# Kernel tuning notes

Measured on AMD Instinct MI355X. Metric: run time of the kernel, lower is better.

## Reference

```python
import jax, jax.numpy as jnp
import numpy as np

B, T, C = 2, 2048, 1024
H = 16
HD = C // H  # 64


def setup_inputs() -> dict:
    key = jax.random.key(0)
    k1, k2, k3, k4, k5 = jax.random.split(key, 5)
    s = 0.02
    return {
        "x": jax.random.normal(k1, (B, T, C), dtype=jnp.float32),
        "w_attn": jax.random.normal(k2, (C, 3 * C), dtype=jnp.float32) * s,
        "b_attn": jnp.zeros((3 * C,), dtype=jnp.float32),
        "w_proj": jax.random.normal(k3, (C, C), dtype=jnp.float32) * s,
        "b_proj": jnp.zeros((C,), dtype=jnp.float32),
    }


def reference(x, w_attn, b_attn, w_proj, b_proj):
    Bx, Tx, Cx = x.shape
    qkv = x @ w_attn + b_attn                      # [B,T,3C]
    q, k, v = jnp.split(qkv, 3, axis=-1)
    # [B,T,C] -> [B,H,T,HD]
    def heads(t):
        return t.reshape(Bx, Tx, H, HD).transpose(0, 2, 1, 3)
    q, k, v = heads(q), heads(k), heads(v)
    scale = 1.0 / np.sqrt(HD).astype(np.float32)
    scores = jnp.einsum("bhqd,bhkd->bhqk", q, k) * scale
    causal = jnp.tril(jnp.ones((Tx, Tx), dtype=bool))
    scores = jnp.where(causal, scores, -jnp.inf)
    attn = jax.nn.softmax(scores, axis=-1)          # dropout p=0 -> identity
    y = jnp.einsum("bhqk,bhkd->bhqd", attn, v)
    y = y.transpose(0, 2, 1, 3).reshape(Bx, Tx, Cx)
    return y @ w_proj + b_proj
```

## Files before the change

kernel.cpp:

```cpp
#include <hip/hip_runtime.h>
#include <hip/hip_bf16.h>

#define Bb 2
#define Tt 2048
#define Cc 1024
#define Hh 16
#define HD 64
#define QS 0.18033688f

typedef __attribute__((ext_vector_type(8))) short bf16x8;
typedef __attribute__((ext_vector_type(4))) short bf16x4;
typedef __attribute__((ext_vector_type(4))) float f32x4;
typedef __attribute__((ext_vector_type(2))) unsigned int u32x2;

__device__ inline short f2b(float f) {
    unsigned int u = __builtin_bit_cast(unsigned int, f);
    unsigned int r = (u + 0x7FFFu + ((u >> 16) & 1u)) >> 16;
    return (short)(unsigned short)r;
}

__device__ inline void gl16(const void* g, void* l) {
    __builtin_amdgcn_global_load_lds(
        (const __attribute__((address_space(1))) void*)g,
        (__attribute__((address_space(3))) void*)l, 16, 0, 0);
}

__global__ __launch_bounds__(256) void prep_kernel(
    const float* __restrict__ x, short* __restrict__ xbf,
    const float* __restrict__ wA, short* __restrict__ wAT,
    const float* __restrict__ wP, short* __restrict__ wPT)
{
    const int bx = blockIdx.x, tid = threadIdx.x;
    if (bx < 2048) {
        int i = (bx * 256 + tid) * 8;
        float4 a = *(const float4*)(x + i);
        float4 b = *(const float4*)(x + i + 4);
        bf16x8 v;
        v[0] = f2b(a.x); v[1] = f2b(a.y); v[2] = f2b(a.z); v[3] = f2b(a.w);
        v[4] = f2b(b.x); v[5] = f2b(b.y); v[6] = f2b(b.z); v[7] = f2b(b.w);
        *(bf16x8*)(xbf + i) = v;
        return;
    }
    const float* W; short* WT; int N, t;
    if (bx < 2816) { t = bx - 2048; W = wA; WT = wAT; N = 3072; }
    else           { t = bx - 2816; W = wP; WT = wPT; N = 1024; }
    const int K = 1024;
    int k0 = (t & 15) * 64, n0 = (t >> 4) * 64;
    int nl = tid & 63, kg = tid >> 6;
    int n = n0 + nl;
    short v[16];
#pragma unroll
    for (int i = 0; i < 16; i++)
        v[i] = f2b(W[(size_t)(k0 + kg * 16 + i) * N + n]);
    short* dst = WT + (size_t)n * K + k0 + kg * 16;
    *(bf16x8*)dst = *(bf16x8*)&v[0];
    *(bf16x8*)(dst + 8) = *(bf16x8*)&v[8];
}

#define VM0 asm volatile("s_waitcnt vmcnt(0)" ::: "memory")
#define BARRIER asm volatile("s_barrier" ::: "memory")
#define SCHEDB __builtin_amdgcn_sched_barrier(0)

#define STG(nb, kb) { \
    gl16(A + baA0 + (kb), &LB[((nb) << 1) * 4096 + dst8]); \
    gl16(A + baA0 + 32768 + (kb), &LB[((nb) << 1) * 4096 + 2048 + dst8]); \
    gl16(A + baA1 + (kb), &LB[(((nb) << 1) | 1) * 4096 + dst8]); \
    gl16(A + baA1 + 32768 + (kb), &LB[(((nb) << 1) | 1) * 4096 + 2048 + dst8]); \
    gl16(Bt + baB0 + (kb), &LB[16384 + ((nb) << 1) * 4096 + dst8]); \
    gl16(Bt + baB0 + 32768 + (kb), &LB[16384 + ((nb) << 1) * 4096 + 2048 + dst8]); \
    gl16(Bt + baB1 + (kb), &LB[16384 + (((nb) << 1) | 1) * 4096 + dst8]); \
    gl16(Bt + baB1 + 32768 + (kb), &LB[16384 + (((nb) << 1) | 1) * 4096 + 2048 + dst8]); }

#define RD_A(bb, flo) { \
    const short* Ab_ = &LB[(((bb) << 1) | wm) * 4096]; \
    _Pragma("unroll") for (int f_ = 0; f_ < 2; f_++) \
        _Pragma("unroll") for (int kh_ = 0; kh_ < 2; kh_++) \
            af[(flo) + f_][kh_] = *(const bf16x8*)&Ab_[aro[(flo) + f_] + kx[kh_]]; }

#define RD_B(bb, elo) { \
    const short* Bb_ = &LB[16384 + (((bb) << 1) | wn) * 4096]; \
    _Pragma("unroll") for (int e_ = 0; e_ < 2; e_++) \
        _Pragma("unroll") for (int kh_ = 0; kh_ < 2; kh_++) \
            bf[(elo) + e_][kh_] = *(const bf16x8*)&Bb_[bro[(elo) + e_] + kx[kh_]]; }

#define QMM(FH, EH) { \
    __builtin_amdgcn_s_setprio(1); \
    _Pragma("unroll") for (int f_ = 0; f_ < 2; f_++) \
        _Pragma("unroll") for (int e_ = 0; e_ < 2; e_++) \
            _Pragma("unroll") for (int kh_ = 0; kh_ < 2; kh_++) \
                acc[(FH) * 2 + f_][(EH) * 2 + e_] = \
                    __builtin_amdgcn_mfma_f32_16x16x32_bf16( \
                        af[(FH) * 2 + f_][kh_], bf[(EH) * 2 + e_][kh_], \
                        acc[(FH) * 2 + f_][(EH) * 2 + e_], 0, 0, 0); \
    __builtin_amdgcn_s_setprio(0); }

#define TILE(bb, nb, kb1) { \
    RD_A(bb, 0); RD_B(bb, 0); \
    STG(nb, kb1); \
    QMM(0, 0); \
    RD_B(bb, 2); QMM(0, 1); \
    RD_A(bb, 2); QMM(1, 1); \
    QMM(1, 0); \
    VM0; BARRIER; SCHEDB; }

#define TILE_LAST(bb) { \
    RD_A(bb, 0); RD_B(bb, 0); \
    QMM(0, 0); \
    RD_B(bb, 2); QMM(0, 1); \
    RD_A(bb, 2); QMM(1, 1); \
    QMM(1, 0); }

__global__ __launch_bounds__(256, 2) void gemm_qkv(
    const short* __restrict__ A, const short* __restrict__ Bt,
    const float* __restrict__ bias,
    short* __restrict__ qw, short* __restrict__ kw, short* __restrict__ vTw,
    int M, int N, int K)
{
    __shared__ __attribute__((aligned(16))) short LB[32768];

    const int tid  = threadIdx.x;
    const int wave = tid >> 6, lane = tid & 63;
    const int quad = lane >> 4, lr = lane & 15;
    const int wm = wave >> 1, wn = wave & 1;

    const int bid = blockIdx.x;
    const int sw = (bid & 7) * 96 + (bid >> 3);
    const int bx = sw % 24, by = sw / 24;
    const int m0 = by * 128, n0 = bx * 128;

    const int dst8 = tid * 8;
    const int cs = ((tid & 7) ^ ((tid >> 3) & 7)) << 3;
    const size_t baA0 = (size_t)(m0 + (tid >> 3)) * 1024 + cs;
    const size_t baA1 = (size_t)(m0 + 64 + (tid >> 3)) * 1024 + cs;
    const size_t baB0 = (size_t)(n0 + (tid >> 3)) * 1024 + cs;
    const size_t baB1 = (size_t)(n0 + 64 + (tid >> 3)) * 1024 + cs;

    int aro[4], bro[4], kx[2];
#pragma unroll
    for (int f = 0; f < 4; f++) {
        aro[f] = (f * 16 + lr) * 64;
        bro[f] = (f * 16 + lr) * 64;
    }
#pragma unroll
    for (int kh = 0; kh < 2; kh++)
        kx[kh] = (((kh * 4 + quad) ^ (lr & 7)) << 3);

    f32x4 acc[4][4];
    const f32x4 zf = {0.f, 0.f, 0.f, 0.f};
#pragma unroll
    for (int mf = 0; mf < 4; mf++)
#pragma unroll
        for (int nf = 0; nf < 4; nf++) acc[mf][nf] = zf;

    bf16x8 af[4][2], bf[4][2];

    STG(0, 0);
    VM0;
    BARRIER;

    for (int it = 0; it < 7; ++it) {
        TILE(0, 1, (2 * it + 1) << 6);
        TILE(1, 0, (2 * it + 2) << 6);
    }
    TILE(0, 1, 15 << 6);
    TILE_LAST(1);

    if (n0 < 2048) {
#pragma unroll
        for (int nf = 0; nf < 4; nf++) {
#pragma unroll
            for (int mf = 0; mf < 4; mf++) {
                int c = n0 + wn * 64 + nf * 16 + lr;
                float bv = bias[c];
#pragma unroll
                for (int r = 0; r < 4; r++) {
                    int rg = m0 + wm * 64 + mf * 16 + quad * 4 + r;
                    float val = acc[mf][nf][r] + bv;
                    int which = c >> 10, cc = c & 1023;
                    int h = cc >> 6, d = cc & 63;
                    int b = rg >> 11, t = rg & 2047;
                    size_t bh = (size_t)b * Hh + h;
                    if (which == 0) qw[(bh * Tt + t) * HD + d] = f2b(val * QS);
                    else            kw[(bh * Tt + t) * HD + d] = f2b(val);
                }
            }
        }
    } else {
        __syncthreads();
#pragma unroll
        for (int nf = 0; nf < 4; nf++) {
            int cl = wn * 64 + nf * 16 + lr;
            float bv = bias[n0 + cl];
#pragma unroll
            for (int mf = 0; mf < 4; mf++)
#pragma unroll
                for (int r = 0; r < 4; r++) {
                    int tl = wm * 64 + mf * 16 + quad * 4 + r;
                    LB[cl * 136 + tl] = f2b(acc[mf][nf][r] + bv);
                }
        }
        __syncthreads();
        const int rl = tid >> 1, half = tid & 1;
        const int cc = (n0 & 1023) + rl;
        const int h = cc >> 6, d = cc & 63;
        const int b = m0 >> 11, tb = (m0 & 2047) + half * 64;
        short* dst = vTw + (((size_t)b * Hh + h) * HD + d) * Tt + tb;
        const short* src = &LB[rl * 136 + half * 64];
#pragma unroll
        for (int jj = 0; jj < 8; jj++)
            *(bf16x8*)(dst + jj * 8) = *(const bf16x8*)(src + jj * 8);
    }
}

__global__ __launch_bounds__(256) void gemm_proj(
    const short* __restrict__ A, const short* __restrict__ Bt,
    const float* __restrict__ bias, float* __restrict__ out,
    int M, int N, int K)
{
    __shared__ __attribute__((aligned(16))) short SH[12288];

    const int tid  = threadIdx.x;
    const int wave = tid >> 6, lane = tid & 63;
    const int quad = lane >> 4, lr = lane & 15;
    const int wm = wave >> 1, wn = wave & 1;
    const int m0 = blockIdx.y * 64, n0 = blockIdx.x * 128;

    const int arow = tid >> 2;
    const int acol = ((tid & 3) ^ ((arow >> 1) & 3)) << 3;
    int brow[2], bcol[2];
#pragma unroll
    for (int i = 0; i < 2; i++) {
        int id = i * 256 + tid;
        brow[i] = id >> 2;
        bcol[i] = ((id & 3) ^ ((brow[i] >> 1) & 3)) << 3;
    }
    const int pfrag = quad ^ ((lr >> 1) & 3);

    f32x4 acc[2][4];
    const f32x4 zf = {0.f, 0.f, 0.f, 0.f};
#pragma unroll
    for (int mi = 0; mi < 2; mi++)
#pragma unroll
        for (int ni = 0; ni < 4; ni++) acc[mi][ni] = zf;

    auto asrc = [&](int row, int col) -> const short* {
        int rg = m0 + row, b = rg >> 11, t = rg & 2047;
        int h = col >> 6, d = col & 63;
        return A + ((((size_t)b * Hh + h) * Tt + t) * HD + d);
    };

    gl16(asrc(arow, acol), &SH[tid * 8]);
#pragma unroll
    for (int i = 0; i < 2; i++)
        gl16(Bt + (size_t)(n0 + brow[i]) * K + bcol[i],
             &SH[4096 + (i * 256 + tid) * 8]);

    const int iters = K >> 5;
    for (int it = 0; it < iters; ++it) {
        const int coA = (it & 1) * 2048, noA = ((it & 1) ^ 1) * 2048;
        const int coB = (it & 1) * 4096, noB = ((it & 1) ^ 1) * 4096;
        __syncthreads();
        if (it + 1 < iters) {
            const int k1 = (it + 1) << 5;
            gl16(asrc(arow, k1 + acol), &SH[noA + tid * 8]);
#pragma unroll
            for (int i = 0; i < 2; i++)
                gl16(Bt + (size_t)(n0 + brow[i]) * K + k1 + bcol[i],
                     &SH[4096 + noB + (i * 256 + tid) * 8]);
        }
        bf16x8 af[2], bf[4];
#pragma unroll
        for (int mi = 0; mi < 2; mi++) {
            int row = wm * 32 + mi * 16 + lr;
            af[mi] = *(bf16x8*)&SH[coA + (row * 4 + pfrag) * 8];
        }
#pragma unroll
        for (int ni = 0; ni < 4; ni++) {
            int row = wn * 64 + ni * 16 + lr;
            bf[ni] = *(bf16x8*)&SH[4096 + coB + (row * 4 + pfrag) * 8];
        }
#pragma unroll
        for (int mi = 0; mi < 2; mi++)
#pragma unroll
            for (int ni = 0; ni < 4; ni++)
                acc[mi][ni] = __builtin_amdgcn_mfma_f32_16x16x32_bf16(
                    af[mi], bf[ni], acc[mi][ni], 0, 0, 0);
    }

#pragma unroll
    for (int mi = 0; mi < 2; mi++)
#pragma unroll
        for (int ni = 0; ni < 4; ni++) {
            int c = n0 + wn * 64 + ni * 16 + lr;
            float bv = bias[c];
#pragma unroll
            for (int r = 0; r < 4; r++) {
                int rg = m0 + wm * 32 + mi * 16 + quad * 4 + r;
                out[(size_t)rg * N + c] = acc[mi][ni][r] + bv;
            }
        }
}

__global__ __launch_bounds__(256) void gemm_f32src(
    const void* __restrict__ Araw, const float* __restrict__ Bm,
    const float* __restrict__ bias, float* __restrict__ out,
    short* __restrict__ qw, short* __restrict__ kw, short* __restrict__ vTw,
    int M, int N, int K, int mode)
{
    __shared__ __attribute__((aligned(16))) short As[128 * 32];
    __shared__ __attribute__((aligned(16))) short Bs[128 * 32];

    const int tid  = threadIdx.x;
    const int wave = tid >> 6, lane = tid & 63;
    const int quad = lane >> 4, lr = lane & 15;
    const int wm = wave >> 1, wn = wave & 1;
    const int m0 = blockIdx.y * 128, n0 = blockIdx.x * 128;

    f32x4 acc[4][4];
    const f32x4 zf = {0.f, 0.f, 0.f, 0.f};
#pragma unroll
    for (int mi = 0; mi < 4; mi++)
#pragma unroll
        for (int ni = 0; ni < 4; ni++) acc[mi][ni] = zf;

    for (int k0 = 0; k0 < K; k0 += 32) {
        __syncthreads();
        if (mode == 1) {
            const float* Af = (const float*)Araw;
#pragma unroll
            for (int i = 0; i < 4; i++) {
                int id  = i * 256 + tid;
                int row = id >> 3;
                int kc  = (id & 7) << 2;
                float4 v = *(const float4*)(Af + (size_t)(m0 + row) * K + k0 + kc);
                short* d = &As[row * 32 + kc];
                d[0] = f2b(v.x); d[1] = f2b(v.y); d[2] = f2b(v.z); d[3] = f2b(v.w);
            }
        } else {
            const short* Ah = (const short*)Araw;
#pragma unroll
            for (int i = 0; i < 2; i++) {
                int id  = i * 256 + tid;
                int row = id >> 2;
                int kc  = (id & 3) << 3;
                int rg = m0 + row, b = rg >> 11, t = rg & 2047;
                int c = k0 + kc, h = c >> 6, d = c & 63;
                *(bf16x8*)&As[row * 32 + kc] =
                    *(const bf16x8*)(Ah + ((((size_t)b * Hh + h) * Tt + t) * HD + d));
            }
        }
#pragma unroll
        for (int i = 0; i < 4; i++) {
            int id = i * 256 + tid;
            int kr = id >> 5;
            int nc = (id & 31) << 2;
            float4 v = *(const float4*)(Bm + (size_t)(k0 + kr) * N + n0 + nc);
            Bs[(nc + 0) * 32 + kr] = f2b(v.x);
            Bs[(nc + 1) * 32 + kr] = f2b(v.y);
            Bs[(nc + 2) * 32 + kr] = f2b(v.z);
            Bs[(nc + 3) * 32 + kr] = f2b(v.w);
        }
        __syncthreads();

        bf16x8 af[4], bf[4];
#pragma unroll
        for (int mi = 0; mi < 4; mi++)
            af[mi] = *(bf16x8*)&As[(wm * 64 + mi * 16 + lr) * 32 + quad * 8];
#pragma unroll
        for (int ni = 0; ni < 4; ni++)
            bf[ni] = *(bf16x8*)&Bs[(wn * 64 + ni * 16 + lr) * 32 + quad * 8];
#pragma unroll
        for (int mi = 0; mi < 4; mi++)
#pragma unroll
            for (int ni = 0; ni < 4; ni++)
                acc[mi][ni] = __builtin_amdgcn_mfma_f32_16x16x32_bf16(
                    af[mi], bf[ni], acc[mi][ni], 0, 0, 0);
    }

#pragma unroll
    for (int mi = 0; mi < 4; mi++) {
#pragma unroll
        for (int ni = 0; ni < 4; ni++) {
            int c = n0 + wn * 64 + ni * 16 + lr;
            float bv = bias[c];
#pragma unroll
            for (int r = 0; r < 4; r++) {
                int rg = m0 + wm * 64 + mi * 16 + quad * 4 + r;
                float val = acc[mi][ni][r] + bv;
                if (mode == 1) {
                    int which = c >> 10, cc = c & 1023;
                    int h = cc >> 6, d = cc & 63;
                    int b = rg >> 11, t = rg & 2047;
                    size_t bh = (size_t)b * Hh + h;
                    if (which == 0)      qw[(bh * Tt + t) * HD + d] = f2b(val * QS);
                    else if (which == 1) kw[(bh * Tt + t) * HD + d] = f2b(val);
                    else                 vTw[(bh * HD + d) * Tt + t] = f2b(val);
                } else {
                    out[(size_t)rg * N + c] = val;
                }
            }
        }
    }
}

__global__ __launch_bounds__(256) void attn_kernel(
    short* __restrict__ qw, const short* __restrict__ kw,
    const short* __restrict__ vTw)
{
    __shared__ __attribute__((aligned(16))) short Ks[2][8192];
    __shared__ __attribute__((aligned(16))) short Vs[2][8192];

    const int bh = blockIdx.x & 31;
    const int g  = blockIdx.x >> 5;
    const int tid = threadIdx.x;
    const int wave = tid >> 6, lane = tid & 63;
    const int quad = lane >> 4, lr = lane & 15;

    const int pA = 2 * g + (wave >> 1);
    const int pB = 63 - pA;
    const int wh = (wave & 1) * 16;
    const int r0m[2] = { pA * 32 + wh, pB * 32 + wh };

    short* qp = qw + (size_t)bh * Tt * HD;
    const short* kp = kw + (size_t)bh * Tt * HD;
    const short* vp = vTw + (size_t)bh * HD * Tt;

    int krow[4], kcol[4], vrow[4], vcol[4];
#pragma unroll
    for (int i = 0; i < 4; i++) {
        int id = i * 256 + tid;
        krow[i] = id >> 3;
        kcol[i] = ((id & 7) ^ (krow[i] & 7)) << 3;
        vrow[i] = id >> 4;
        vcol[i] = ((id & 15) ^ (vrow[i] & 15)) << 3;
    }

    const int kb0b = lr * 64 + ((quad     ^ (lr & 7)) << 3);
    const int kb1b = lr * 64 + (((4 + quad) ^ (lr & 7)) << 3);
    const int qh = quad >> 1, ql = quad & 1;
    int vbase[4];
#pragma unroll
    for (int nt = 0; nt < 4; nt++)
        vbase[nt] = (nt * 16 + lr) * 128 + ql * 4;

    bf16x8 aq[2][2];
#pragma unroll
    for (int mt = 0; mt < 2; mt++)
#pragma unroll
        for (int h = 0; h < 2; h++)
            aq[mt][h] = *(const bf16x8*)(qp + (size_t)(r0m[mt] + lr) * HD
                                            + h * 32 + quad * 8);

    const f32x4 zf = {0.f, 0.f, 0.f, 0.f};
    f32x4 o[2][4];
    float lacc[2] = {0.f, 0.f};
#pragma unroll
    for (int mt = 0; mt < 2; mt++)
#pragma unroll
        for (int nt = 0; nt < 4; nt++) o[mt][nt] = zf;

#pragma unroll
    for (int i = 0; i < 4; i++) {
        gl16(kp + (size_t)krow[i] * HD + kcol[i], &Ks[0][(i * 256 + tid) * 8]);
        gl16(vp + (size_t)vrow[i] * Tt + vcol[i], &Vs[0][(i * 256 + tid) * 8]);
    }

    const int clast = ((63 - 2 * g) * 32 + 31) >> 7;
    for (int c = 0; c <= clast; ++c) {
        const int j0 = c << 7;
        const int cur = c & 1;
        __syncthreads();
        if (c < clast) {
#pragma unroll
            for (int i = 0; i < 4; i++) {
                gl16(kp + (size_t)(j0 + 128 + krow[i]) * HD + kcol[i],
                     &Ks[cur ^ 1][(i * 256 + tid) * 8]);
                gl16(vp + (size_t)vrow[i] * Tt + (j0 + 128) + vcol[i],
                     &Vs[cur ^ 1][(i * 256 + tid) * 8]);
            }
        }
        const short* Kc = &Ks[cur][0];
        const short* Vc = &Vs[cur][0];
        __builtin_amdgcn_s_setprio(1);
#pragma unroll
        for (int kt = 0; kt < 8; kt++) {
            const int k16 = j0 + kt * 16;
            const bool act0 = k16 <= r0m[0] + 15;
            const bool act1 = k16 <= r0m[1] + 15;
            if (!act1 && !act0) break;
            bf16x8 kb0 = *(const bf16x8*)&Kc[kt * 1024 + kb0b];
            bf16x8 kb1 = *(const bf16x8*)&Kc[kt * 1024 + kb1b];
            const int sl8 = (((kt * 2 + qh) ^ lr) << 3);
            bf16x4 va[4];
#pragma unroll
            for (int nt = 0; nt < 4; nt++)
                va[nt] = *(const bf16x4*)&Vc[vbase[nt] + sl8];
#pragma unroll
            for (int mt = 0; mt < 2; mt++) {
                if (!(mt ? act1 : act0)) continue;
                f32x4 s = __builtin_amdgcn_mfma_f32_16x16x32_bf16(
                    kb0, aq[mt][0], zf, 0, 0, 0);
                s = __builtin_amdgcn_mfma_f32_16x16x32_bf16(
                    kb1, aq[mt][1], s, 0, 0, 0);
                unsigned u[4];
                if (k16 + 15 <= r0m[mt]) {
#pragma unroll
                    for (int r = 0; r < 4; r++) {
                        float e = __builtin_amdgcn_exp2f(s[r]);
                        u[r] = __builtin_bit_cast(unsigned, e);
                        lacc[mt] += e;
                    }
                } else {
#pragma unroll
                    for (int r = 0; r < 4; r++) {
                        float e = __builtin_amdgcn_exp2f(s[r]);
                        if ((k16 + quad * 4 + r) > (r0m[mt] + lr)) e = 0.f;
                        u[r] = __builtin_bit_cast(unsigned, e);
                        lacc[mt] += e;
                    }
                }
                u32x2 pu = { __builtin_amdgcn_perm(u[1], u[0], 0x07060302u),
                             __builtin_amdgcn_perm(u[3], u[2], 0x07060302u) };
                bf16x4 pt = __builtin_bit_cast(bf16x4, pu);
#pragma unroll
                for (int nt = 0; nt < 4; nt++)
                    o[mt][nt] = __builtin_amdgcn_mfma_f32_16x16x16bf16_1k(
                        va[nt], pt, o[mt][nt], 0, 0, 0);
            }
        }
        __builtin_amdgcn_s_setprio(0);
    }

#pragma unroll
    for (int mt = 0; mt < 2; mt++) {
        lacc[mt] += __shfl_xor(lacc[mt], 16, 64);
        lacc[mt] += __shfl_xor(lacc[mt], 32, 64);
        lacc[mt] = 1.0f / lacc[mt];
    }

#pragma unroll
    for (int mt = 0; mt < 2; mt++)
#pragma unroll
        for (int nt = 0; nt < 4; nt++) {
            bf16x4 ov;
#pragma unroll
            for (int r = 0; r < 4; r++) ov[r] = f2b(o[mt][nt][r] * lacc[mt]);
            *(bf16x4*)(qp + (size_t)(r0m[mt] + lr) * HD + nt * 16 + quad * 4) = ov;
        }
}

extern "C" void kernel_launch(void* const* d_in, const int* in_sizes, int n_in,
                              void* d_out, int out_size, void* d_ws, size_t ws_size,
                              hipStream_t stream) {
    const float* x      = (const float*)d_in[0];
    const float* w_attn = (const float*)d_in[1];
    const float* b_attn = (const float*)d_in[2];
    const float* w_proj = (const float*)d_in[3];
    const float* b_proj = (const float*)d_in[4];
    float* out = (float*)d_out;

    const size_t per = (size_t)Bb * Hh * Tt * HD;
    short* qw  = (short*)d_ws;
    short* kw  = qw + per;
    short* vTw = kw + per;
    const int M = Bb * Tt;

    const size_t need_fast = (3 * per + per + (size_t)3072 * 1024 + (size_t)1024 * 1024) * 2;

    if (ws_size >= need_fast) {
        short* xbf = vTw + per;
        short* wAT = xbf + per;
        short* wPT = wAT + (size_t)3072 * 1024;

        prep_kernel<<<dim3(3072), 256, 0, stream>>>(x, xbf, w_attn, wAT, w_proj, wPT);

        gemm_qkv<<<dim3(768), 256, 0, stream>>>(
            xbf, wAT, b_attn, qw, kw, vTw, M, 3 * Cc, Cc);

        attn_kernel<<<dim3(512), 256, 0, stream>>>(qw, kw, vTw);

        gemm_proj<<<dim3(Cc / 128, M / 64), 256, 0, stream>>>(
            qw, wPT, b_proj, out, M, Cc, Cc);
    } else {
        gemm_f32src<<<dim3(3 * Cc / 128, M / 128), 256, 0, stream>>>(
            x, w_attn, b_attn, nullptr, qw, kw, vTw, M, 3 * Cc, Cc, 1);

        attn_kernel<<<dim3(512), 256, 0, stream>>>(qw, kw, vTw);

        gemm_f32src<<<dim3(Cc / 128, M / 128), 256, 0, stream>>>(
            qw, w_proj, b_proj, out, nullptr, nullptr, nullptr, M, Cc, Cc, 2);
    }
}
```

Measured before the change: 174.9 us.

## Split attention key tiles across two wave groups and pipeline proj GEMM with K=64 tiles

The attention kernel now runs 512 threads per block: two groups of four waves each handle half of every 128-key chunk. Their partial outputs and row sums are combined through shared memory at the end. This doubles the waves per query tile, aiming to cut per-wave serial latency, at the cost of a final reduction and fewer load instructions per thread. The projection GEMM is rewritten to use K=64 tiles in a macro-driven double-buffered loop with interleaved LDS reads and MFMAs, priority hints and launch_bounds(256,2), which trades more shared memory for fewer barriers.

Result: no change. 171.5 us (-1.9%).

```diff
diff --git a/kernel.cpp b/kernel.cpp
--- a/kernel.cpp
+++ b/kernel.cpp
@@ -212,12 +212,55 @@
     }
 }
 
-__global__ __launch_bounds__(256) void gemm_proj(
+#define P_STG(nb, kb) { \
+    gl16(A + baA0 + (size_t)(kb) * 2048, &LB[(nb) * 4096 + dst8]); \
+    gl16(A + baA1 + (size_t)(kb) * 2048, &LB[(nb) * 4096 + 2048 + dst8]); \
+    gl16(Bt + baB0 + (kb), &LB[8192 + (nb) * 8192 + dst8]); \
+    gl16(Bt + baB1 + (kb), &LB[8192 + (nb) * 8192 + 2048 + dst8]); \
+    gl16(Bt + baB2 + (kb), &LB[8192 + (nb) * 8192 + 4096 + dst8]); \
+    gl16(Bt + baB3 + (kb), &LB[8192 + (nb) * 8192 + 6144 + dst8]); }
+
+#define P_RDA(bb) { \
+    const short* Ab_ = &LB[(bb) * 4096]; \
+    _Pragma("unroll") for (int f_ = 0; f_ < 2; f_++) \
+        _Pragma("unroll") for (int kh_ = 0; kh_ < 2; kh_++) \
+            af[f_][kh_] = *(const bf16x8*)&Ab_[aro[f_] + kx[kh_]]; }
+
+#define P_RDB(bb, elo) { \
+    const short* Bb_ = &LB[8192 + (bb) * 8192]; \
+    _Pragma("unroll") for (int e_ = 0; e_ < 2; e_++) \
+        _Pragma("unroll") for (int kh_ = 0; kh_ < 2; kh_++) \
+            bf[(elo) + e_][kh_] = *(const bf16x8*)&Bb_[bro[(elo) + e_] + kx[kh_]]; }
+
+#define P_QMM(EH) { \
+    __builtin_amdgcn_s_setprio(1); \
+    _Pragma("unroll") for (int f_ = 0; f_ < 2; f_++) \
+        _Pragma("unroll") for (int e_ = 0; e_ < 2; e_++) \
+            _Pragma("unroll") for (int kh_ = 0; kh_ < 2; kh_++) \
+                acc[f_][(EH) * 2 + e_] = \
+                    __builtin_amdgcn_mfma_f32_16x16x32_bf16( \
+                        af[f_][kh_], bf[(EH) * 2 + e_][kh_], \
+                        acc[f_][(EH) * 2 + e_], 0, 0, 0); \
+    __builtin_amdgcn_s_setprio(0); }
+
+#define P_TILE(bb, nb, kb1) { \
+    P_RDA(bb); P_RDB(bb, 0); \
+    P_STG(nb, kb1); \
+    P_QMM(0); \
+    P_RDB(bb, 2); P_QMM(1); \
+    VM0; BARRIER; SCHEDB; }
+
+#define P_TILE_LAST(bb) { \
+    P_RDA(bb); P_RDB(bb, 0); \
+    P_QMM(0); \
+    P_RDB(bb, 2); P_QMM(1); }
+
+__global__ __launch_bounds__(256, 2) void gemm_proj(
     const short* __restrict__ A, const short* __restrict__ Bt,
     const float* __restrict__ bias, float* __restrict__ out,
     int M, int N, int K)
 {
-    __shared__ __attribute__((aligned(16))) short SH[12288];
+    __shared__ __attribute__((aligned(16))) short LB[24576];
 
     const int tid  = threadIdx.x;
     const int wave = tid >> 6, lane = tid & 63;
@@ -225,16 +268,27 @@
     const int wm = wave >> 1, wn = wave & 1;
     const int m0 = blockIdx.y * 64, n0 = blockIdx.x * 128;
 
-    const int arow = tid >> 2;
-    const int acol = ((tid & 3) ^ ((arow >> 1) & 3)) << 3;
-    int brow[2], bcol[2];
-#pragma unroll
-    for (int i = 0; i < 2; i++) {
-        int id = i * 256 + tid;
-        brow[i] = id >> 2;
-        bcol[i] = ((id & 3) ^ ((brow[i] >> 1) & 3)) << 3;
-    }
-    const int pfrag = quad ^ ((lr >> 1) & 3);
+    const int dst8 = tid * 8;
+    const int cs = ((tid & 7) ^ ((tid >> 3) & 7)) << 3;
+    size_t baA0, baA1;
+    {
+        int r0 = m0 + (tid >> 3), r1 = m0 + 32 + (tid >> 3);
+        baA0 = (((size_t)(r0 >> 11) * Hh) * Tt + (r0 & 2047)) * HD + cs;
+        baA1 = (((size_t)(r1 >> 11) * Hh) * Tt + (r1 & 2047)) * HD + cs;
+    }
+    const size_t baB0 = (size_t)(n0 + (tid >> 3)) * 1024 + cs;
+    const size_t baB1 = (size_t)(n0 + 32 + (tid >> 3)) * 1024 + cs;
+    const size_t baB2 = (size_t)(n0 + 64 + (tid >> 3)) * 1024 + cs;
+    const size_t baB3 = (size_t)(n0 + 96 + (tid >> 3)) * 1024 + cs;
+
+    int aro[2], bro[4], kx[2];
+#pragma unroll
+    for (int f = 0; f < 2; f++) aro[f] = (wm * 32 + f * 16 + lr) * 64;
+#pragma unroll
+    for (int e = 0; e < 4; e++) bro[e] = (wn * 64 + e * 16 + lr) * 64;
+#pragma unroll
+    for (int kh = 0; kh < 2; kh++)
+        kx[kh] = (((kh * 4 + quad) ^ (lr & 7)) << 3);
 
     f32x4 acc[2][4];
     const f32x4 zf = {0.f, 0.f, 0.f, 0.f};
@@ -243,49 +297,18 @@
 #pragma unroll
         for (int ni = 0; ni < 4; ni++) acc[mi][ni] = zf;
 
-    auto asrc = [&](int row, int col) -> const short* {
-        int rg = m0 + row, b = rg >> 11, t = rg & 2047;
-        int h = col >> 6, d = col & 63;
-        return A + ((((size_t)b * Hh + h) * Tt + t) * HD + d);
-    };
-
-    gl16(asrc(arow, acol), &SH[tid * 8]);
-#pragma unroll
-    for (int i = 0; i < 2; i++)
-        gl16(Bt + (size_t)(n0 + brow[i]) * K + bcol[i],
-             &SH[4096 + (i * 256 + tid) * 8]);
-
-    const int iters = K >> 5;
-    for (int it = 0; it < iters; ++it) {
-        const int coA = (it & 1) * 2048, noA = ((it & 1) ^ 1) * 2048;
-        const int coB = (it & 1) * 4096, noB = ((it & 1) ^ 1) * 4096;
-        __syncthreads();
-        if (it + 1 < iters) {
-            const int k1 = (it + 1) << 5;
-            gl16(asrc(arow, k1 + acol), &SH[noA + tid * 8]);
-#pragma unroll
-            for (int i = 0; i < 2; i++)
-                gl16(Bt + (size_t)(n0 + brow[i]) * K + k1 + bcol[i],
-                     &SH[4096 + noB + (i * 256 + tid) * 8]);
-        }
-        bf16x8 af[2], bf[4];
-#pragma unroll
-        for (int mi = 0; mi < 2; mi++) {
-            int row = wm * 32 + mi * 16 + lr;
-            af[mi] = *(bf16x8*)&SH[coA + (row * 4 + pfrag) * 8];
-        }
-#pragma unroll
-        for (int ni = 0; ni < 4; ni++) {
-            int row = wn * 64 + ni * 16 + lr;
-            bf[ni] = *(bf16x8*)&SH[4096 + coB + (row * 4 + pfrag) * 8];
-        }
-#pragma unroll
-        for (int mi = 0; mi < 2; mi++)
-#pragma unroll
-            for (int ni = 0; ni < 4; ni++)
-                acc[mi][ni] = __builtin_amdgcn_mfma_f32_16x16x32_bf16(
-                    af[mi], bf[ni], acc[mi][ni], 0, 0, 0);
-    }
+    bf16x8 af[2][2], bf[4][2];
+
+    P_STG(0, 0);
+    VM0;
+    BARRIER;
+
+    for (int it = 0; it < 7; ++it) {
+        P_TILE(0, 1, (2 * it + 1) << 6);
+        P_TILE(1, 0, (2 * it + 2) << 6);
+    }
+    P_TILE(0, 1, 15 << 6);
+    P_TILE_LAST(1);
 
 #pragma unroll
     for (int mi = 0; mi < 2; mi++)
@@ -403,7 +426,7 @@
     }
 }
 
-__global__ __launch_bounds__(256) void attn_kernel(
+__global__ __launch_bounds__(512) void attn_kernel(
     short* __restrict__ qw, const short* __restrict__ kw,
     const short* __restrict__ vTw)
 {
@@ -414,21 +437,22 @@
     const int g  = blockIdx.x >> 5;
     const int tid = threadIdx.x;
     const int wave = tid >> 6, lane = tid & 63;
+    const int wg = wave & 3, kgrp = wave >> 2;
     const int quad = lane >> 4, lr = lane & 15;
 
-    const int pA = 2 * g + (wave >> 1);
+    const int pA = 2 * g + (wg >> 1);
     const int pB = 63 - pA;
-    const int wh = (wave & 1) * 16;
+    const int wh = (wg & 1) * 16;
     const int r0m[2] = { pA * 32 + wh, pB * 32 + wh };
 
     short* qp = qw + (size_t)bh * Tt * HD;
     const short* kp = kw + (size_t)bh * Tt * HD;
     const short* vp = vTw + (size_t)bh * HD * Tt;
 
-    int krow[4], kcol[4], vrow[4], vcol[4];
-#pragma unroll
-    for (int i = 0; i < 4; i++) {
-        int id = i * 256 + tid;
+    int krow[2], kcol[2], vrow[2], vcol[2];
+#pragma unroll
+    for (int i = 0; i < 2; i++) {
+        int id = i * 512 + tid;
         krow[i] = id >> 3;
         kcol[i] = ((id & 7) ^ (krow[i] & 7)) << 3;
         vrow[i] = id >> 4;
@@ -460,9 +484,9 @@
         for (int nt = 0; nt < 4; nt++) o[mt][nt] = zf;
 
 #pragma unroll
-    for (int i = 0; i < 4; i++) {
-        gl16(kp + (size_t)krow[i] * HD + kcol[i], &Ks[0][(i * 256 + tid) * 8]);
-        gl16(vp + (size_t)vrow[i] * Tt + vcol[i], &Vs[0][(i * 256 + tid) * 8]);
+    for (int i = 0; i < 2; i++) {
+        gl16(kp + (size_t)krow[i] * HD + kcol[i], &Ks[0][(i * 512 + tid) * 8]);
+        gl16(vp + (size_t)vrow[i] * Tt + vcol[i], &Vs[0][(i * 512 + tid) * 8]);
     }
 
     const int clast = ((63 - 2 * g) * 32 + 31) >> 7;
@@ -472,18 +496,19 @@
         __syncthreads();
         if (c < clast) {
 #pragma unroll
-            for (int i = 0; i < 4; i++) {
+            for (int i = 0; i < 2; i++) {
                 gl16(kp + (size_t)(j0 + 128 + krow[i]) * HD + kcol[i],
-                     &Ks[cur ^ 1][(i * 256 + tid) * 8]);
+                     &Ks[cur ^ 1][(i * 512 + tid) * 8]);
                 gl16(vp + (size_t)vrow[i] * Tt + (j0 + 128) + vcol[i],
-                     &Vs[cur ^ 1][(i * 256 + tid) * 8]);
+                     &Vs[cur ^ 1][(i * 512 + tid) * 8]);
             }
         }
         const short* Kc = &Ks[cur][0];
         const short* Vc = &Vs[cur][0];
         __builtin_amdgcn_s_setprio(1);
 #pragma unroll
-        for (int kt = 0; kt < 8; kt++) {
+        for (int k4 = 0; k4 < 4; k4++) {
+            const int kt = kgrp * 4 + k4;
             const int k16 = j0 + kt * 16;
             const bool act0 = k16 <= r0m[0] + 15;
             const bool act1 = k16 <= r0m[1] + 15;
@@ -531,22 +556,48 @@
         __builtin_amdgcn_s_setprio(0);
     }
 
-#pragma unroll
-    for (int mt = 0; mt < 2; mt++) {
-        lacc[mt] += __shfl_xor(lacc[mt], 16, 64);
-        lacc[mt] += __shfl_xor(lacc[mt], 32, 64);
-        lacc[mt] = 1.0f / lacc[mt];
-    }
-
-#pragma unroll
-    for (int mt = 0; mt < 2; mt++)
-#pragma unroll
-        for (int nt = 0; nt < 4; nt++) {
-            bf16x4 ov;
-#pragma unroll
-            for (int r = 0; r < 4; r++) ov[r] = f2b(o[mt][nt][r] * lacc[mt]);
-            *(bf16x4*)(qp + (size_t)(r0m[mt] + lr) * HD + nt * 16 + quad * 4) = ov;
-        }
+    __syncthreads();
+    float* po = (float*)&Ks[0][0];
+    float* pl = (float*)&Vs[0][0];
+    if (kgrp) {
+#pragma unroll
+        for (int mt = 0; mt < 2; mt++)
+#pragma unroll
+            for (int nt = 0; nt < 4; nt++)
+                *(f32x4*)&po[(wg * 64 + lane) * 32 + (mt * 4 + nt) * 4] = o[mt][nt];
+        pl[(wg * 64 + lane) * 2 + 0] = lacc[0];
+        pl[(wg * 64 + lane) * 2 + 1] = lacc[1];
+    }
+    __syncthreads();
+    if (kgrp == 0) {
+#pragma unroll
+        for (int mt = 0; mt < 2; mt++)
+#pragma unroll
+            for (int nt = 0; nt < 4; nt++) {
+                f32x4 t = *(const f32x4*)&po[(wg * 64 + lane) * 32 + (mt * 4 + nt) * 4];
+#pragma unroll
+                for (int r = 0; r < 4; r++) o[mt][nt][r] += t[r];
+            }
+        lacc[0] += pl[(wg * 64 + lane) * 2 + 0];
+        lacc[1] += pl[(wg * 64 + lane) * 2 + 1];
+
+#pragma unroll
+        for (int mt = 0; mt < 2; mt++) {
+            lacc[mt] += __shfl_xor(lacc[mt], 16, 64);
+            lacc[mt] += __shfl_xor(lacc[mt], 32, 64);
+            lacc[mt] = 1.0f / lacc[mt];
+        }
+
+#pragma unroll
+        for (int mt = 0; mt < 2; mt++)
+#pragma unroll
+            for (int nt = 0; nt < 4; nt++) {
+                bf16x4 ov;
+#pragma unroll
+                for (int r = 0; r < 4; r++) ov[r] = f2b(o[mt][nt][r] * lacc[mt]);
+                *(bf16x4*)(qp + (size_t)(r0m[mt] + lr) * HD + nt * 16 + quad * 4) = ov;
+            }
+    }
 }
 
 extern "C" void kernel_launch(void* const* d_in, const int* in_sizes, int n_in,
@@ -577,7 +628,7 @@
         gemm_qkv<<<dim3(768), 256, 0, stream>>>(
             xbf, wAT, b_attn, qw, kw, vTw, M, 3 * Cc, Cc);
 
-        attn_kernel<<<dim3(512), 256, 0, stream>>>(qw, kw, vTw);
+        attn_kernel<<<dim3(512), 512, 0, stream>>>(qw, kw, vTw);
 
         gemm_proj<<<dim3(Cc / 128, M / 64), 256, 0, stream>>>(
             qw, wPT, b_proj, out, M, Cc, Cc);
@@ -585,7 +636,7 @@
         gemm_f32src<<<dim3(3 * Cc / 128, M / 128), 256, 0, stream>>>(
             x, w_attn, b_attn, nullptr, qw, kw, vTw, M, 3 * Cc, Cc, 1);
 
-        attn_kernel<<<dim3(512), 256, 0, stream>>>(qw, kw, vTw);
+        attn_kernel<<<dim3(512), 512, 0, stream>>>(qw, kw, vTw);
 
         gemm_f32src<<<dim3(Cc / 128, M / 128), 256, 0, stream>>>(
             qw, w_proj, b_proj, out, nullptr, nullptr, nullptr, M, Cc, Cc, 2);
```
